# Kernel optimization log

Hardware: AMD Instinct MI355X
Metric: run time of the kernel (lower is better)

## Reference

```python
import jax, jax.numpy as jnp
import numpy as np

B, S, HID, NH, KCLIP = 2, 1500, 1024, 16, 64
HD = HID // NH  # 64


def setup_inputs() -> dict:
    key = jax.random.key(0)
    ks = jax.random.split(key, 16)
    std = 0.02
    inp = {
        "query": jax.random.normal(ks[0], (B, S, HID), jnp.float32),
        "key": jax.random.normal(ks[1], (B, S, HID), jnp.float32),
        "value": jax.random.normal(ks[2], (B, S, HID), jnp.float32),
        # per-head projection weights, stacked over heads: [NH, HID, HD]
        "Wq": jax.random.normal(ks[3], (NH, HID, HD), jnp.float32) * std,
        "bq": jax.random.normal(ks[4], (NH, HD), jnp.float32) * std,
        "Wk": jax.random.normal(ks[5], (NH, HID, HD), jnp.float32) * std,
        "bk": jax.random.normal(ks[6], (NH, HD), jnp.float32) * std,
        "Wv": jax.random.normal(ks[7], (NH, HID, HD), jnp.float32) * std,
        "bv": jax.random.normal(ks[8], (NH, HD), jnp.float32) * std,
        # Shaw relative-position embedding tables: [2k+1, HD]
        "pe_k": jax.random.normal(ks[9], (2 * KCLIP + 1, HD), jnp.float32) * std,
        "pe_v": jax.random.normal(ks[10], (2 * KCLIP + 1, HD), jnp.float32) * std,
        # output projection (torch Linear stored as x @ W + b here)
        "W_fc": jax.random.normal(ks[11], (HID, HID), jnp.float32) * std,
        "b_fc": jax.random.normal(ks[12], (HID,), jnp.float32) * std,
    }
    return inp


def _rel_bias(pe, length, k_clip):
    idx = jnp.arange(length)
    dist = jnp.clip(idx[None, :] - idx[:, None], -k_clip, k_clip) + k_clip
    return pe[dist]  # [S, S, HD]


def reference(query, key, value, Wq, bq, Wk, bk, Wv, bv, pe_k, pe_v, W_fc, b_fc):
    head_dim = Wq.shape[-1]
    seq = query.shape[1]
    k_clip = (pe_k.shape[0] - 1) // 2

    kb = _rel_bias(pe_k, seq, k_clip)  # [S, S, HD]
    vb = _rel_bias(pe_v, seq, k_clip)  # [S, S, HD]

    # batched per-head projections: [B, NH, S, HD]
    Q = jnp.einsum('bsh,nhd->bnsd', query, Wq) + bq[None, :, None, :]
    K = jnp.einsum('bsh,nhd->bnsd', key, Wk) + bk[None, :, None, :]
    V = jnp.einsum('bsh,nhd->bnsd', value, Wv) + bv[None, :, None, :]

    # content term + Shaw relative-key bias term
    scores = jnp.einsum('bnqd,bnkd->bnqk', Q, K) \
           + jnp.einsum('bnqd,qkd->bnqk', Q, kb)
    scores = scores / jnp.sqrt(jnp.asarray(head_dim, scores.dtype))

    w = jax.nn.softmax(scores, axis=-1)  # [B, NH, S, S]

    out = jnp.einsum('bnqk,bnkd->bnqd', w, V) \
        + jnp.einsum('bnqk,qkd->bnqd', w, vb)

    # concat heads (head order matches ModuleList concatenation)
    hidden = out.transpose(0, 2, 1, 3).reshape(query.shape[0], seq, -1)
    return hidden @ W_fc + b_fc
```

## Files before the change

### kernel.cpp

```cpp
#include <hip/hip_runtime.h>
#include <math.h>

#define B_     2
#define S_     1500
#define HID_   1024
#define NH_    16
#define HD_    64
#define M_     (B_*S_)
#define SP_    1536
#define LOG2E  1.4426950408889634f

typedef short bf16x8 __attribute__((ext_vector_type(8)));
typedef short bf16x4 __attribute__((ext_vector_type(4)));
typedef float f32x4  __attribute__((ext_vector_type(4)));

__device__ __forceinline__ float b2f(short s) {
    unsigned u = ((unsigned)(unsigned short)s) << 16;
    return __uint_as_float(u);
}
__device__ __forceinline__ short f2b(float f) {
    unsigned u = __float_as_uint(f);
    unsigned r = (u + 0x7FFFu + ((u >> 16) & 1u)) >> 16;
    return (short)r;
}
__device__ __forceinline__ void gload16(const short* src, short* lds) {
    __builtin_amdgcn_global_load_lds(
        (const __attribute__((address_space(1))) void*)src,
        (__attribute__((address_space(3))) void*)lds, 16, 0, 0);
}

__global__ __launch_bounds__(256) void cvt_act3(
    const float* __restrict__ q, const float* __restrict__ k,
    const float* __restrict__ v, short* __restrict__ oq,
    short* __restrict__ ok, short* __restrict__ ov)
{
    const float* src = blockIdx.y == 0 ? q : blockIdx.y == 1 ? k : v;
    short* dst       = blockIdx.y == 0 ? oq : blockIdx.y == 1 ? ok : ov;
    int i = blockIdx.x * 256 + threadIdx.x;
    const float4* p = (const float4*)(src + (size_t)i * 8);
    float4 a = p[0], b = p[1];
    bf16x8 o;
    o[0]=f2b(a.x); o[1]=f2b(a.y); o[2]=f2b(a.z); o[3]=f2b(a.w);
    o[4]=f2b(b.x); o[5]=f2b(b.y); o[6]=f2b(b.z); o[7]=f2b(b.w);
    *(bf16x8*)(dst + (size_t)i * 8) = o;
}

__global__ __launch_bounds__(256) void prep_w(
    const float* __restrict__ Wq, const float* __restrict__ Wk,
    const float* __restrict__ Wv, const float* __restrict__ Wfc,
    const float* __restrict__ pe_k, const float* __restrict__ pe_v,
    short* __restrict__ Wqt, short* __restrict__ Wkt, short* __restrict__ Wvt,
    short* __restrict__ Wfh, short* __restrict__ Wfl,
    short* __restrict__ pe_kb, short* __restrict__ pe_vt)
{
    int z = blockIdx.x, tid = threadIdx.x;
    if (z == 1024) {
        for (int s = tid; s < 144 * 64; s += 256) {
            int j = s >> 6, d = s & 63;
            pe_kb[s] = (j < 129) ? f2b(pe_k[j * 64 + d]) : (short)0;
        }
        for (int s = tid; s < 64 * 160; s += 256) {
            int d = s / 160, j = s - d * 160;
            pe_vt[s] = (j < 129) ? f2b(pe_v[j * 64 + d]) : (short)0;
        }
        return;
    }
    __shared__ float T[64][65];
    const float* src; short* dhi; short* dlo = nullptr;
    int C, c0, r0; float scale = 1.f;
    if (z < 768) {
        int widx = z >> 8, rem = z & 255;
        int h = rem >> 4, rt = rem & 15;
        src = (widx == 0 ? Wq : widx == 1 ? Wk : Wv) + (size_t)h * 1024 * 64;
        dhi = (widx == 0 ? Wqt : widx == 1 ? Wkt : Wvt) + (size_t)h * 64 * 1024;
        scale = (widx == 0) ? 0.125f * LOG2E : 1.0f;
        C = 64; c0 = 0; r0 = rt * 64;
    } else {
        int idx = z - 768;
        src = Wfc; dhi = Wfh; dlo = Wfl;
        C = 1024; c0 = (idx >> 4) * 64; r0 = (idx & 15) * 64;
    }
#pragma unroll
    for (int i = 0; i < 4; ++i) {
        int slot = tid + i * 256;
        int r = slot >> 4, cg = (slot & 15) * 4;
        float4 v = *(const float4*)(src + (size_t)(r0 + r) * C + c0 + cg);
        T[r][cg+0] = v.x*scale; T[r][cg+1] = v.y*scale;
        T[r][cg+2] = v.z*scale; T[r][cg+3] = v.w*scale;
    }
    __syncthreads();
#pragma unroll
    for (int i = 0; i < 16; ++i) {
        int slot = tid + i * 256;
        int c = slot >> 6, r = slot & 63;
        float v = T[r][c];
        short hi = f2b(v);
        size_t o = (size_t)(c0 + c) * 1024 + r0 + r;
        dhi[o] = hi;
        if (dlo) dlo[o] = f2b(v - b2f(hi));
    }
}

__device__ __forceinline__ void gemm_core(
    const short* __restrict__ Ahi, const short* __restrict__ Alo,
    const short* __restrict__ Bhi, const short* __restrict__ Blo,
    int kIters, int m0, int n0, short* As, short* Bs, f32x4 (&acc)[4][4])
{
    const int tid = threadIdx.x, w = tid >> 6, lane = tid & 63;
    const int l15 = lane & 15, lr4 = lane >> 4;
    const int wr = w >> 1, wc = w & 1;

    for (int it = 0; it < kIters; ++it) {
        int kt = it * 64;
        int seg = kt >> 10, kk0 = kt & 1023;
        const short* Aseg = (seg == 1) ? Alo : Ahi;
        const short* Bseg = (seg == 2) ? Blo : Bhi;
        __syncthreads();
#pragma unroll
        for (int c = 0; c < 4; ++c) {
            int slot = (w * 4 + c) * 64 + lane;
            int r = slot >> 3, cb = slot & 7;
            int sm = m0 + r; sm = sm < M_ ? sm : M_ - 1;
            gload16(Aseg + (size_t)sm * 1024 + kk0 + ((cb ^ (r & 7)) * 8),
                    As + (size_t)(w * 4 + c) * 512);
            gload16(Bseg + (size_t)(n0 + r) * 1024 + kk0 + ((cb ^ (r & 7)) * 8),
                    Bs + (size_t)(w * 4 + c) * 512);
        }
        __syncthreads();
#pragma unroll
        for (int kh = 0; kh < 2; ++kh) {
            bf16x8 aF[4], bF[4];
#pragma unroll
            for (int mi = 0; mi < 4; ++mi) {
                int r = wr * 64 + mi * 16 + l15;
                aF[mi] = *(const bf16x8*)(As + r * 64 + (((kh*4+lr4) ^ (r & 7)) * 8));
            }
#pragma unroll
            for (int ni = 0; ni < 4; ++ni) {
                int r = wc * 64 + ni * 16 + l15;
                bF[ni] = *(const bf16x8*)(Bs + r * 64 + (((kh*4+lr4) ^ (r & 7)) * 8));
            }
#pragma unroll
            for (int mi = 0; mi < 4; ++mi)
#pragma unroll
                for (int ni = 0; ni < 4; ++ni)
                    acc[mi][ni] = __builtin_amdgcn_mfma_f32_16x16x32_bf16(
                        aF[mi], bF[ni], acc[mi][ni], 0, 0, 0);
        }
    }
}

__global__ __launch_bounds__(256) void gemm_qkv(
    const short* __restrict__ qb, const short* __restrict__ kb,
    const short* __restrict__ vb, const short* __restrict__ Wqt,
    const short* __restrict__ Wkt, const short* __restrict__ Wvt,
    const float* __restrict__ bq, const float* __restrict__ bk,
    const float* __restrict__ bv,
    short* __restrict__ Qp, short* __restrict__ Kp, short* __restrict__ Vp)
{
    __shared__ short As[128 * 64];
    __shared__ short Bs[128 * 64];
    const int z = blockIdx.z;
    const short* A  = z == 0 ? qb : z == 1 ? kb : vb;
    const short* Bw = z == 0 ? Wqt : z == 1 ? Wkt : Wvt;
    const float* bias = z == 0 ? bq : z == 1 ? bk : bv;
    const float bscale = z == 0 ? 0.125f * LOG2E : 1.0f;
    short* out = z == 0 ? Qp : z == 1 ? Kp : Vp;
    const int m0 = blockIdx.x * 128, n0 = blockIdx.y * 128;

    f32x4 zf = {0.f,0.f,0.f,0.f};
    f32x4 acc[4][4];
#pragma unroll
    for (int i = 0; i < 4; ++i)
#pragma unroll
        for (int j = 0; j < 4; ++j) acc[i][j] = zf;

    gemm_core(A, A, Bw, Bw, 16, m0, n0, As, Bs, acc);

    const int tid = threadIdx.x, w = tid >> 6, lane = tid & 63;
    const int l15 = lane & 15, lr4 = lane >> 4;
    const int wr = w >> 1, wc = w & 1;
#pragma unroll
    for (int mi = 0; mi < 4; ++mi)
#pragma unroll
        for (int rr = 0; rr < 4; ++rr) {
            int m = m0 + wr * 64 + mi * 16 + lr4 * 4 + rr;
            if (m >= M_) continue;
            int b = m / S_, s = m - b * S_;
#pragma unroll
            for (int ni = 0; ni < 4; ++ni) {
                int n = n0 + wc * 64 + ni * 16 + l15;
                float v = acc[mi][ni][rr] + bias[n] * bscale;
                int h = n >> 6, d = n & 63;
                out[(((size_t)(b * NH_ + h)) * S_ + s) * HD_ + d] = f2b(v);
            }
        }
}

__global__ __launch_bounds__(256) void gemm_fc(
    const short* __restrict__ Ahi, const short* __restrict__ Alo,
    const short* __restrict__ Bhi, const short* __restrict__ Blo,
    const float* __restrict__ bias, float* __restrict__ out)
{
    __shared__ short As[128 * 64];
    __shared__ short Bs[128 * 64];
    const int m0 = blockIdx.x * 128, n0 = blockIdx.y * 128;
    f32x4 zf = {0.f,0.f,0.f,0.f};
    f32x4 acc[4][4];
#pragma unroll
    for (int i = 0; i < 4; ++i)
#pragma unroll
        for (int j = 0; j < 4; ++j) acc[i][j] = zf;

    gemm_core(Ahi, Alo, Bhi, Blo, 32, m0, n0, As, Bs, acc);

    const int tid = threadIdx.x, w = tid >> 6, lane = tid & 63;
    const int l15 = lane & 15, lr4 = lane >> 4;
    const int wr = w >> 1, wc = w & 1;
#pragma unroll
    for (int mi = 0; mi < 4; ++mi)
#pragma unroll
        for (int rr = 0; rr < 4; ++rr) {
            int m = m0 + wr * 64 + mi * 16 + lr4 * 4 + rr;
            if (m >= M_) continue;
#pragma unroll
            for (int ni = 0; ni < 4; ++ni) {
                int n = n0 + wc * 64 + ni * 16 + l15;
                out[(size_t)m * 1024 + n] = acc[mi][ni][rr] + bias[n];
            }
        }
}

__global__ __launch_bounds__(256) void vtrans(
    const short* __restrict__ Vp, short* __restrict__ Vtg)
{
    __shared__ short T[64][72];
    const int bh = blockIdx.y, s0 = blockIdx.x * 64, tid = threadIdx.x;
    const size_t kv = (size_t)bh * S_ * 64;
#pragma unroll
    for (int i = 0; i < 2; ++i) {
        int slot = tid + i * 256;
        int r = slot >> 3, cb = slot & 7;
        int ss = s0 + r; ss = ss < S_ ? ss : S_ - 1;
        bf16x8 v = *(const bf16x8*)(Vp + kv + (size_t)ss * 64 + cb * 8);
        *(bf16x8*)(&T[r][cb * 8]) = v;
    }
    __syncthreads();
#pragma unroll
    for (int i = 0; i < 2; ++i) {
        int slot = tid + i * 256;
        int d = slot >> 3, cg = slot & 7;
        bf16x8 v;
#pragma unroll
        for (int j = 0; j < 8; ++j) {
            int kk = 32 * (cg >> 2) + ((j >> 2) & 1) * 16 + (cg & 3) * 4 + (j & 3);
            v[j] = T[kk][d];
        }
        *(bf16x8*)(Vtg + ((size_t)bh * 64 + d) * SP_ + s0 + cg * 8) = v;
    }
}

__global__ __launch_bounds__(256, 4) void attn_mfma(
    const short* __restrict__ Qb, const short* __restrict__ Kb,
    const short* __restrict__ Vtg, const short* __restrict__ pe_kb,
    const short* __restrict__ pe_vt,
    short* __restrict__ hid_hi, short* __restrict__ hid_lo)
{
    __shared__ short qpe[64 * 144];
    __shared__ short wsm[64 * 160];

    const int tid = threadIdx.x, w = tid >> 6, lane = tid & 63;
    const int l15 = lane & 15, lr4 = lane >> 4;
    const int lg = (blockIdx.x & 7) * 96 + (blockIdx.x >> 3);
    const int bh = lg / 24, bx = lg - bh * 24;
    const int q0 = bx * 64;
    const int qw = q0 + w * 16;
    const int myq = qw + l15;
    const int myrow = w * 16 + l15;
    const size_t kv  = (size_t)bh * S_ * HD_;
    const size_t vtb = (size_t)bh * 64 * SP_;

    {
        short ini = f2b(-1e30f);
        bf16x8 iv;
#pragma unroll
        for (int i = 0; i < 8; ++i) iv[i] = ini;
        short* base = wsm + w * 16 * 160;
#pragma unroll
        for (int i = 0; i < 5; ++i)
            *(bf16x8*)(base + (size_t)(i * 64 + lane) * 8) = iv;
    }

    bf16x8 qA[2];
    {
        int sq = myq < S_ ? myq : S_ - 1;
        const short* qp = Qb + kv + (size_t)sq * 64 + lr4 * 8;
        qA[0] = *(const bf16x8*)(qp);
        qA[1] = *(const bf16x8*)(qp + 32);
    }

    f32x4 zf = {0.f,0.f,0.f,0.f};
#pragma unroll
    for (int jt = 0; jt < 9; ++jt) {
        f32x4 a = zf;
#pragma unroll
        for (int kh = 0; kh < 2; ++kh) {
            bf16x8 pf = *(const bf16x8*)(pe_kb + (size_t)(jt * 16 + l15) * 64 + kh * 32 + lr4 * 8);
            a = __builtin_amdgcn_mfma_f32_16x16x32_bf16(pf, qA[kh], a, 0, 0, 0);
        }
        bf16x4 pk;
#pragma unroll
        for (int rr = 0; rr < 4; ++rr) pk[rr] = f2b(a[rr]);
        *(bf16x4*)(qpe + (size_t)myrow * 144 + jt * 16 + lr4 * 4) = pk;
    }
    const float qpe0   = b2f(qpe[myrow * 144 + 0]);
    const float qpe128 = b2f(qpe[myrow * 144 + 128]);

    float m = 0.f, s0s = 0.f, s1s = 0.f;
    f32x4 o[4];
#pragma unroll
    for (int t = 0; t < 4; ++t) o[t] = zf;

    for (int c = 0; c < 12; ++c) {
        const int kc = c * 128;

        const bool lo0 = (kc +  63 - qw) <= -64, hi0 = (kc       - (qw + 15)) >= 64;
        const bool lo1 = (kc + 127 - qw) <= -64, hi1 = (kc + 64  - (qw + 15)) >= 64;
        const bool mx0 = !(lo0 || hi0), mx1 = !(lo1 || hi1);
        const float ub0 = lo0 ? qpe0 : qpe128;
        const float ub1 = lo1 ? qpe0 : qpe128;

        float rm = -1e30f;
        bf16x8 pa[2][2];
#pragma unroll
        for (int t8 = 0; t8 < 8; ++t8) {
            int sk = kc + t8 * 16 + l15; sk = sk < S_ ? sk : S_ - 1;
            const short* kp = Kb + kv + (size_t)sk * 64 + lr4 * 8;
            bf16x8 k0 = *(const bf16x8*)(kp);
            bf16x8 k1 = *(const bf16x8*)(kp + 32);
            f32x4 s = __builtin_amdgcn_mfma_f32_16x16x32_bf16(k0, qA[0], zf, 0, 0, 0);
            s = __builtin_amdgcn_mfma_f32_16x16x32_bf16(k1, qA[1], s, 0, 0, 0);

            const int h = t8 >> 2, tt = t8 & 3;
            const int wn = tt >> 1, sl = (tt & 1) * 4;
            const bool mx = h ? mx1 : mx0;
            const bool alo = h ? lo1 : lo0;
            const float ub = h ? ub1 : ub0;
#pragma unroll
            for (int rr = 0; rr < 4; ++rr) {
                int k = kc + t8 * 16 + lr4 * 4 + rr;
                int rel = k - myq;
                float v;
                if (mx) {
                    int jc = rel < -64 ? 0 : (rel > 64 ? 128 : rel + 64);
                    v = s[rr] + b2f(qpe[myrow * 144 + jc]);
                } else {
                    v = s[rr] + ub;
                }
                if (k >= S_) v = -1e30f;
                rm = fmaxf(rm, v);
                if (mx && rel > -64 && rel < 64)
                    wsm[myrow * 160 + rel + 64] = f2b(v);
                float p2 = exp2f(v - m);
                pa[h][wn][sl + rr] = f2b(p2);
                if (mx) {
                    if (rel <= -64) s0s += p2; else if (rel >= 64) s1s += p2;
                } else if (alo) s0s += p2; else s1s += p2;
            }
        }

        __builtin_amdgcn_s_setprio(1);
#pragma unroll
        for (int h = 0; h < 2; ++h)
#pragma unroll
            for (int wn = 0; wn < 2; ++wn)
#pragma unroll
                for (int td = 0; td < 4; ++td) {
                    int r = td * 16 + l15;
                    int cbv = h * 8 + wn * 4 + lr4;
                    bf16x8 vB = *(const bf16x8*)(Vtg + vtb + (size_t)r * SP_ + kc + cbv * 8);
                    o[td] = __builtin_amdgcn_mfma_f32_16x16x32_bf16(pa[h][wn], vB, o[td], 0, 0, 0);
                }
        __builtin_amdgcn_s_setprio(0);

        rm = fmaxf(rm, __shfl_xor(rm, 16));
        rm = fmaxf(rm, __shfl_xor(rm, 32));
        if (!__all(rm <= m + 8.f)) {
            float nm = fmaxf(m, rm);
            float fac = exp2f(m - nm);
            m = nm; s0s *= fac; s1s *= fac;
            float fo[4];
#pragma unroll
            for (int rr = 0; rr < 4; ++rr) fo[rr] = __shfl(fac, lr4 * 4 + rr);
#pragma unroll
            for (int t = 0; t < 4; ++t)
#pragma unroll
                for (int rr = 0; rr < 4; ++rr) o[t][rr] *= fo[rr];
        }
    }

    s0s += __shfl_xor(s0s, 16); s0s += __shfl_xor(s0s, 32);
    s1s += __shfl_xor(s1s, 16); s1s += __shfl_xor(s1s, 32);

    short* rowp = wsm + (size_t)myrow * 160;
    float midsum = 0.f;
#pragma unroll
    for (int cc = 0; cc < 5; ++cc) {
        int off = (cc * 4 + lr4) * 8;
        bf16x8 mv = *(const bf16x8*)(rowp + off);
        bf16x8 ev;
#pragma unroll
        for (int jj = 0; jj < 8; ++jj) {
            float e = exp2f(b2f(mv[jj]) - m);
            ev[jj] = f2b(e);
            midsum += e;
        }
        *(bf16x8*)(rowp + off) = ev;
    }
    midsum += __shfl_xor(midsum, 16); midsum += __shfl_xor(midsum, 32);
    const float linv = 1.f / (s0s + s1s + midsum);
    if (lr4 == 0) { rowp[0] = f2b(s0s); rowp[128] = f2b(s1s); }

#pragma unroll
    for (int jh = 0; jh < 5; ++jh) {
        bf16x8 aW = *(const bf16x8*)(wsm + (size_t)myrow * 160 + jh * 32 + lr4 * 8);
#pragma unroll
        for (int td = 0; td < 4; ++td) {
            bf16x8 bW = *(const bf16x8*)(pe_vt + (size_t)(td * 16 + l15) * 160 + jh * 32 + lr4 * 8);
            o[td] = __builtin_amdgcn_mfma_f32_16x16x32_bf16(aW, bW, o[td], 0, 0, 0);
        }
    }

    {
        float fo[4];
#pragma unroll
        for (int rr = 0; rr < 4; ++rr) fo[rr] = __shfl(linv, lr4 * 4 + rr);
#pragma unroll
        for (int td = 0; td < 4; ++td)
#pragma unroll
            for (int rr = 0; rr < 4; ++rr) o[td][rr] *= fo[rr];
    }

#pragma unroll
    for (int td = 0; td < 4; ++td)
#pragma unroll
        for (int rr = 0; rr < 4; ++rr) {
            int qrow = lr4 * 4 + rr;
            int d = td * 16 + l15;
            int inner = (((d >> 2) ^ ((qrow & 7) << 1)) << 2) + (d & 3);
            float v = o[td][rr];
            short hi = f2b(v);
            wsm[(w * 16 + qrow) * 160 + inner] = hi;
            qpe[(w * 16 + qrow) * 144 + inner] = f2b(v - b2f(hi));
        }
    {
        int b = bh >> 4, h = bh & 15;
        int qrow = lane >> 2;
        int q = q0 + w * 16 + qrow;
#pragma unroll
        for (int i = 0; i < 2; ++i) {
            int cb = (lane & 3) * 2 + i;
            int qws = (cb * 2) ^ ((qrow & 7) << 1);
            bf16x8 hv = *(const bf16x8*)(wsm + (w * 16 + qrow) * 160 + qws * 4);
            bf16x8 lv = *(const bf16x8*)(qpe + (w * 16 + qrow) * 144 + qws * 4);
            if (q < S_) {
                size_t oo = ((size_t)(b * S_ + q)) * 1024 + h * 64 + cb * 8;
                *(bf16x8*)(hid_hi + oo) = hv;
                *(bf16x8*)(hid_lo + oo) = lv;
            }
        }
    }
}

extern "C" void kernel_launch(void* const* d_in, const int* in_sizes, int n_in,
                              void* d_out, int out_size, void* d_ws, size_t ws_size,
                              hipStream_t stream)
{
    const float* query = (const float*)d_in[0];
    const float* key   = (const float*)d_in[1];
    const float* value = (const float*)d_in[2];
    const float* Wq    = (const float*)d_in[3];
    const float* bq    = (const float*)d_in[4];
    const float* Wk    = (const float*)d_in[5];
    const float* bk    = (const float*)d_in[6];
    const float* Wv    = (const float*)d_in[7];
    const float* bv    = (const float*)d_in[8];
    const float* pe_k  = (const float*)d_in[9];
    const float* pe_v  = (const float*)d_in[10];
    const float* W_fc  = (const float*)d_in[11];
    const float* b_fc  = (const float*)d_in[12];

    char* W = (char*)d_ws;
    short* qb   = (short*)(W + 0);
    short* kb   = (short*)(W + 6291456);
    short* vb   = (short*)(W + 12582912);
    short* Vtg  = vb;
    short* Wqt  = (short*)(W + 18874368);
    short* Wkt  = (short*)(W + 20971520);
    short* Wvt  = (short*)(W + 23068672);
    short* Wfh  = (short*)(W + 25165824);
    short* Wfl  = (short*)(W + 27262976);
    short* Qp   = (short*)(W + 29360128);
    short* Kp   = (short*)(W + 35651584);
    short* Vp   = (short*)(W + 41943040);
    short* pekb = (short*)(W + 48234496);
    short* pevt = (short*)(W + 48252928);
    short* hidh = qb;
    short* hidl = kb;

    cvt_act3<<<dim3(1500, 3), 256, 0, stream>>>(query, key, value, qb, kb, vb);
    prep_w<<<1025, 256, 0, stream>>>(Wq, Wk, Wv, W_fc, pe_k, pe_v,
                                     Wqt, Wkt, Wvt, Wfh, Wfl, pekb, pevt);
    gemm_qkv<<<dim3(24, 8, 3), 256, 0, stream>>>(qb, kb, vb, Wqt, Wkt, Wvt,
                                                 bq, bk, bv, Qp, Kp, Vp);
    vtrans<<<dim3(24, 32), 256, 0, stream>>>(Vp, Vtg);
    attn_mfma<<<768, 256, 0, stream>>>(Qp, Kp, Vtg, pekb, pevt, hidh, hidl);
    gemm_fc<<<dim3(24, 8), 256, 0, stream>>>(hidh, hidl, Wfh, Wfl, b_fc, (float*)d_out);
}
```

Measured before the change: 267.0 us.

## Process two 16-row query tiles per wave to reuse K and V fragments

The attention kernel now uses 128-thread blocks where each wave handles 32 query rows as two 16-row MFMA tiles. Each K fragment and V fragment loaded from global memory feeds two MFMAs instead of one, halving K/V load traffic per query. The cost is roughly doubled accumulator and probability registers per wave and fewer waves per block, which may lower occupancy and latency hiding. The launch bounds hint that fixed 4 blocks per CU was also dropped.

```diff
diff --git a/kernel.cpp b/kernel.cpp
--- a/kernel.cpp
+++ b/kernel.cpp
@@ -260,7 +260,7 @@
     }
 }
 
-__global__ __launch_bounds__(256, 4) void attn_mfma(
+__global__ __launch_bounds__(128) void attn_mfma(
     const short* __restrict__ Qb, const short* __restrict__ Kb,
     const short* __restrict__ Vtg, const short* __restrict__ pe_kb,
     const short* __restrict__ pe_vt,
@@ -274,98 +274,125 @@
     const int lg = (blockIdx.x & 7) * 96 + (blockIdx.x >> 3);
     const int bh = lg / 24, bx = lg - bh * 24;
     const int q0 = bx * 64;
-    const int qw = q0 + w * 16;
-    const int myq = qw + l15;
-    const int myrow = w * 16 + l15;
+    const int qwave = q0 + w * 32;
     const size_t kv  = (size_t)bh * S_ * HD_;
     const size_t vtb = (size_t)bh * 64 * SP_;
+
+    int myq[2], myrow[2];
+#pragma unroll
+    for (int t2 = 0; t2 < 2; ++t2) {
+        myq[t2] = qwave + t2 * 16 + l15;
+        myrow[t2] = w * 32 + t2 * 16 + l15;
+    }
 
     {
         short ini = f2b(-1e30f);
         bf16x8 iv;
 #pragma unroll
         for (int i = 0; i < 8; ++i) iv[i] = ini;
-        short* base = wsm + w * 16 * 160;
-#pragma unroll
-        for (int i = 0; i < 5; ++i)
+        short* base = wsm + w * 32 * 160;
+#pragma unroll
+        for (int i = 0; i < 10; ++i)
             *(bf16x8*)(base + (size_t)(i * 64 + lane) * 8) = iv;
     }
 
-    bf16x8 qA[2];
-    {
-        int sq = myq < S_ ? myq : S_ - 1;
+    bf16x8 qA[2][2];
+#pragma unroll
+    for (int t2 = 0; t2 < 2; ++t2) {
+        int sq = myq[t2] < S_ ? myq[t2] : S_ - 1;
         const short* qp = Qb + kv + (size_t)sq * 64 + lr4 * 8;
-        qA[0] = *(const bf16x8*)(qp);
-        qA[1] = *(const bf16x8*)(qp + 32);
+        qA[t2][0] = *(const bf16x8*)(qp);
+        qA[t2][1] = *(const bf16x8*)(qp + 32);
     }
 
     f32x4 zf = {0.f,0.f,0.f,0.f};
 #pragma unroll
-    for (int jt = 0; jt < 9; ++jt) {
-        f32x4 a = zf;
-#pragma unroll
-        for (int kh = 0; kh < 2; ++kh) {
-            bf16x8 pf = *(const bf16x8*)(pe_kb + (size_t)(jt * 16 + l15) * 64 + kh * 32 + lr4 * 8);
-            a = __builtin_amdgcn_mfma_f32_16x16x32_bf16(pf, qA[kh], a, 0, 0, 0);
-        }
-        bf16x4 pk;
-#pragma unroll
-        for (int rr = 0; rr < 4; ++rr) pk[rr] = f2b(a[rr]);
-        *(bf16x4*)(qpe + (size_t)myrow * 144 + jt * 16 + lr4 * 4) = pk;
-    }
-    const float qpe0   = b2f(qpe[myrow * 144 + 0]);
-    const float qpe128 = b2f(qpe[myrow * 144 + 128]);
-
-    float m = 0.f, s0s = 0.f, s1s = 0.f;
-    f32x4 o[4];
-#pragma unroll
-    for (int t = 0; t < 4; ++t) o[t] = zf;
+    for (int t2 = 0; t2 < 2; ++t2)
+#pragma unroll
+        for (int jt = 0; jt < 9; ++jt) {
+            f32x4 a = zf;
+#pragma unroll
+            for (int kh = 0; kh < 2; ++kh) {
+                bf16x8 pf = *(const bf16x8*)(pe_kb + (size_t)(jt * 16 + l15) * 64 + kh * 32 + lr4 * 8);
+                a = __builtin_amdgcn_mfma_f32_16x16x32_bf16(pf, qA[t2][kh], a, 0, 0, 0);
+            }
+            bf16x4 pk;
+#pragma unroll
+            for (int rr = 0; rr < 4; ++rr) pk[rr] = f2b(a[rr]);
+            *(bf16x4*)(qpe + (size_t)myrow[t2] * 144 + jt * 16 + lr4 * 4) = pk;
+        }
+    float qpe0[2], qpe128[2];
+#pragma unroll
+    for (int t2 = 0; t2 < 2; ++t2) {
+        qpe0[t2]   = b2f(qpe[myrow[t2] * 144 + 0]);
+        qpe128[t2] = b2f(qpe[myrow[t2] * 144 + 128]);
+    }
+
+    float m[2] = {0.f, 0.f}, s0s[2] = {0.f, 0.f}, s1s[2] = {0.f, 0.f};
+    f32x4 o[2][4];
+#pragma unroll
+    for (int t2 = 0; t2 < 2; ++t2)
+#pragma unroll
+        for (int t = 0; t < 4; ++t) o[t2][t] = zf;
 
     for (int c = 0; c < 12; ++c) {
         const int kc = c * 128;
 
-        const bool lo0 = (kc +  63 - qw) <= -64, hi0 = (kc       - (qw + 15)) >= 64;
-        const bool lo1 = (kc + 127 - qw) <= -64, hi1 = (kc + 64  - (qw + 15)) >= 64;
-        const bool mx0 = !(lo0 || hi0), mx1 = !(lo1 || hi1);
-        const float ub0 = lo0 ? qpe0 : qpe128;
-        const float ub1 = lo1 ? qpe0 : qpe128;
-
-        float rm = -1e30f;
-        bf16x8 pa[2][2];
+        bool mx[2][2], alo[2][2];
+        float ub[2][2];
+#pragma unroll
+        for (int t2 = 0; t2 < 2; ++t2) {
+            int qt = qwave + t2 * 16;
+#pragma unroll
+            for (int h = 0; h < 2; ++h) {
+                bool lo = (kc + h * 64 + 63 - qt) <= -64;
+                bool hi = (kc + h * 64 - (qt + 15)) >= 64;
+                mx[t2][h] = !(lo || hi);
+                alo[t2][h] = lo;
+                ub[t2][h] = lo ? qpe0[t2] : qpe128[t2];
+            }
+        }
+
+        float rm[2] = {-1e30f, -1e30f};
+        bf16x8 pa[2][2][2];
 #pragma unroll
         for (int t8 = 0; t8 < 8; ++t8) {
             int sk = kc + t8 * 16 + l15; sk = sk < S_ ? sk : S_ - 1;
             const short* kp = Kb + kv + (size_t)sk * 64 + lr4 * 8;
             bf16x8 k0 = *(const bf16x8*)(kp);
             bf16x8 k1 = *(const bf16x8*)(kp + 32);
-            f32x4 s = __builtin_amdgcn_mfma_f32_16x16x32_bf16(k0, qA[0], zf, 0, 0, 0);
-            s = __builtin_amdgcn_mfma_f32_16x16x32_bf16(k1, qA[1], s, 0, 0, 0);
-
             const int h = t8 >> 2, tt = t8 & 3;
             const int wn = tt >> 1, sl = (tt & 1) * 4;
-            const bool mx = h ? mx1 : mx0;
-            const bool alo = h ? lo1 : lo0;
-            const float ub = h ? ub1 : ub0;
-#pragma unroll
-            for (int rr = 0; rr < 4; ++rr) {
-                int k = kc + t8 * 16 + lr4 * 4 + rr;
-                int rel = k - myq;
-                float v;
-                if (mx) {
-                    int jc = rel < -64 ? 0 : (rel > 64 ? 128 : rel + 64);
-                    v = s[rr] + b2f(qpe[myrow * 144 + jc]);
-                } else {
-                    v = s[rr] + ub;
+#pragma unroll
+            for (int t2 = 0; t2 < 2; ++t2) {
+                f32x4 s = __builtin_amdgcn_mfma_f32_16x16x32_bf16(k0, qA[t2][0], zf, 0, 0, 0);
+                s = __builtin_amdgcn_mfma_f32_16x16x32_bf16(k1, qA[t2][1], s, 0, 0, 0);
+                const bool mxx = mx[t2][h];
+                const bool aloo = alo[t2][h];
+                const float ubb = ub[t2][h];
+#pragma unroll
+                for (int rr = 0; rr < 4; ++rr) {
+                    int k = kc + t8 * 16 + lr4 * 4 + rr;
+                    int rel = k - myq[t2];
+                    float v;
+                    if (mxx) {
+                        int jc = rel < -64 ? 0 : (rel > 64 ? 128 : rel + 64);
+                        v = s[rr] + b2f(qpe[myrow[t2] * 144 + jc]);
+                    } else {
+                        v = s[rr] + ubb;
+                    }
+                    if (k >= S_) v = -1e30f;
+                    rm[t2] = fmaxf(rm[t2], v);
+                    if (mxx && rel > -64 && rel < 64)
+                        wsm[myrow[t2] * 160 + rel + 64] = f2b(v);
+                    float p2 = exp2f(v - m[t2]);
+                    pa[t2][h][wn][sl + rr] = f2b(p2);
+                    if (mxx) {
+                        if (rel <= -64) s0s[t2] += p2;
+                        else if (rel >= 64) s1s[t2] += p2;
+                    } else if (aloo) s0s[t2] += p2;
+                    else s1s[t2] += p2;
                 }
-                if (k >= S_) v = -1e30f;
-                rm = fmaxf(rm, v);
-                if (mx && rel > -64 && rel < 64)
-                    wsm[myrow * 160 + rel + 64] = f2b(v);
-                float p2 = exp2f(v - m);
-                pa[h][wn][sl + rr] = f2b(p2);
-                if (mx) {
-                    if (rel <= -64) s0s += p2; else if (rel >= 64) s1s += p2;
-                } else if (alo) s0s += p2; else s1s += p2;
             }
         }
 
@@ -378,95 +405,107 @@
                 for (int td = 0; td < 4; ++td) {
                     int r = td * 16 + l15;
                     int cbv = h * 8 + wn * 4 + lr4;
-                    bf16x8 vB = *(const bf16x8*)(Vtg + vtb + (size_t)r * SP_ + kc + cbv * 8);
-                    o[td] = __builtin_amdgcn_mfma_f32_16x16x32_bf16(pa[h][wn], vB, o[td], 0, 0, 0);
+                    bf16x8 vB = *(const bf16x8*)(
+                        Vtg + vtb + (size_t)r * SP_ + kc + cbv * 8);
+                    o[0][td] = __builtin_amdgcn_mfma_f32_16x16x32_bf16(
+                        pa[0][h][wn], vB, o[0][td], 0, 0, 0);
+                    o[1][td] = __builtin_amdgcn_mfma_f32_16x16x32_bf16(
+                        pa[1][h][wn], vB, o[1][td], 0, 0, 0);
                 }
         __builtin_amdgcn_s_setprio(0);
 
-        rm = fmaxf(rm, __shfl_xor(rm, 16));
-        rm = fmaxf(rm, __shfl_xor(rm, 32));
-        if (!__all(rm <= m + 8.f)) {
-            float nm = fmaxf(m, rm);
-            float fac = exp2f(m - nm);
-            m = nm; s0s *= fac; s1s *= fac;
+#pragma unroll
+        for (int t2 = 0; t2 < 2; ++t2) {
+            float r2 = rm[t2];
+            r2 = fmaxf(r2, __shfl_xor(r2, 16));
+            r2 = fmaxf(r2, __shfl_xor(r2, 32));
+            if (!__all(r2 <= m[t2] + 8.f)) {
+                float nm = fmaxf(m[t2], r2);
+                float fac = exp2f(m[t2] - nm);
+                m[t2] = nm; s0s[t2] *= fac; s1s[t2] *= fac;
+                float fo[4];
+#pragma unroll
+                for (int rr = 0; rr < 4; ++rr) fo[rr] = __shfl(fac, lr4 * 4 + rr);
+#pragma unroll
+                for (int t = 0; t < 4; ++t)
+#pragma unroll
+                    for (int rr = 0; rr < 4; ++rr) o[t2][t][rr] *= fo[rr];
+            }
+        }
+    }
+
+#pragma unroll
+    for (int t2 = 0; t2 < 2; ++t2) {
+        float s0 = s0s[t2], s1 = s1s[t2], mm = m[t2];
+        s0 += __shfl_xor(s0, 16); s0 += __shfl_xor(s0, 32);
+        s1 += __shfl_xor(s1, 16); s1 += __shfl_xor(s1, 32);
+
+        short* rowp = wsm + (size_t)myrow[t2] * 160;
+        float midsum = 0.f;
+#pragma unroll
+        for (int cc = 0; cc < 5; ++cc) {
+            int off = (cc * 4 + lr4) * 8;
+            bf16x8 mv = *(const bf16x8*)(rowp + off);
+            bf16x8 ev;
+#pragma unroll
+            for (int jj = 0; jj < 8; ++jj) {
+                float e = exp2f(b2f(mv[jj]) - mm);
+                ev[jj] = f2b(e);
+                midsum += e;
+            }
+            *(bf16x8*)(rowp + off) = ev;
+        }
+        midsum += __shfl_xor(midsum, 16); midsum += __shfl_xor(midsum, 32);
+        const float linv = 1.f / (s0 + s1 + midsum);
+        if (lr4 == 0) { rowp[0] = f2b(s0); rowp[128] = f2b(s1); }
+
+#pragma unroll
+        for (int jh = 0; jh < 5; ++jh) {
+            bf16x8 aW = *(const bf16x8*)(wsm + (size_t)myrow[t2] * 160 + jh * 32 + lr4 * 8);
+#pragma unroll
+            for (int td = 0; td < 4; ++td) {
+                bf16x8 bW = *(const bf16x8*)(pe_vt + (size_t)(td * 16 + l15) * 160 + jh * 32 + lr4 * 8);
+                o[t2][td] = __builtin_amdgcn_mfma_f32_16x16x32_bf16(aW, bW, o[t2][td], 0, 0, 0);
+            }
+        }
+
+        {
             float fo[4];
 #pragma unroll
-            for (int rr = 0; rr < 4; ++rr) fo[rr] = __shfl(fac, lr4 * 4 + rr);
-#pragma unroll
-            for (int t = 0; t < 4; ++t)
-#pragma unroll
-                for (int rr = 0; rr < 4; ++rr) o[t][rr] *= fo[rr];
-        }
-    }
-
-    s0s += __shfl_xor(s0s, 16); s0s += __shfl_xor(s0s, 32);
-    s1s += __shfl_xor(s1s, 16); s1s += __shfl_xor(s1s, 32);
-
-    short* rowp = wsm + (size_t)myrow * 160;
-    float midsum = 0.f;
-#pragma unroll
-    for (int cc = 0; cc < 5; ++cc) {
-        int off = (cc * 4 + lr4) * 8;
-        bf16x8 mv = *(const bf16x8*)(rowp + off);
-        bf16x8 ev;
-#pragma unroll
-        for (int jj = 0; jj < 8; ++jj) {
-            float e = exp2f(b2f(mv[jj]) - m);
-            ev[jj] = f2b(e);
-            midsum += e;
-        }
-        *(bf16x8*)(rowp + off) = ev;
-    }
-    midsum += __shfl_xor(midsum, 16); midsum += __shfl_xor(midsum, 32);
-    const float linv = 1.f / (s0s + s1s + midsum);
-    if (lr4 == 0) { rowp[0] = f2b(s0s); rowp[128] = f2b(s1s); }
-
-#pragma unroll
-    for (int jh = 0; jh < 5; ++jh) {
-        bf16x8 aW = *(const bf16x8*)(wsm + (size_t)myrow * 160 + jh * 32 + lr4 * 8);
-#pragma unroll
-        for (int td = 0; td < 4; ++td) {
-            bf16x8 bW = *(const bf16x8*)(pe_vt + (size_t)(td * 16 + l15) * 160 + jh * 32 + lr4 * 8);
-            o[td] = __builtin_amdgcn_mfma_f32_16x16x32_bf16(aW, bW, o[td], 0, 0, 0);
-        }
-    }
-
-    {
-        float fo[4];
-#pragma unroll
-        for (int rr = 0; rr < 4; ++rr) fo[rr] = __shfl(linv, lr4 * 4 + rr);
+            for (int rr = 0; rr < 4; ++rr) fo[rr] = __shfl(linv, lr4 * 4 + rr);
+#pragma unroll
+            for (int td = 0; td < 4; ++td)
+#pragma unroll
+                for (int rr = 0; rr < 4; ++rr) o[t2][td][rr] *= fo[rr];
+        }
+
 #pragma unroll
         for (int td = 0; td < 4; ++td)
 #pragma unroll
-            for (int rr = 0; rr < 4; ++rr) o[td][rr] *= fo[rr];
-    }
-
-#pragma unroll
-    for (int td = 0; td < 4; ++td)
-#pragma unroll
-        for (int rr = 0; rr < 4; ++rr) {
-            int qrow = lr4 * 4 + rr;
-            int d = td * 16 + l15;
-            int inner = (((d >> 2) ^ ((qrow & 7) << 1)) << 2) + (d & 3);
-            float v = o[td][rr];
-            short hi = f2b(v);
-            wsm[(w * 16 + qrow) * 160 + inner] = hi;
-            qpe[(w * 16 + qrow) * 144 + inner] = f2b(v - b2f(hi));
-        }
-    {
-        int b = bh >> 4, h = bh & 15;
-        int qrow = lane >> 2;
-        int q = q0 + w * 16 + qrow;
-#pragma unroll
-        for (int i = 0; i < 2; ++i) {
-            int cb = (lane & 3) * 2 + i;
-            int qws = (cb * 2) ^ ((qrow & 7) << 1);
-            bf16x8 hv = *(const bf16x8*)(wsm + (w * 16 + qrow) * 160 + qws * 4);
-            bf16x8 lv = *(const bf16x8*)(qpe + (w * 16 + qrow) * 144 + qws * 4);
-            if (q < S_) {
-                size_t oo = ((size_t)(b * S_ + q)) * 1024 + h * 64 + cb * 8;
-                *(bf16x8*)(hid_hi + oo) = hv;
-                *(bf16x8*)(hid_lo + oo) = lv;
+            for (int rr = 0; rr < 4; ++rr) {
+                int qrow = lr4 * 4 + rr;
+                int d = td * 16 + l15;
+                int inner = (((d >> 2) ^ ((qrow & 7) << 1)) << 2) + (d & 3);
+                float v = o[t2][td][rr];
+                short hi = f2b(v);
+                wsm[(w * 32 + t2 * 16 + qrow) * 160 + inner] = hi;
+                qpe[(w * 32 + t2 * 16 + qrow) * 144 + inner] = f2b(v - b2f(hi));
+            }
+        {
+            int b = bh >> 4, h = bh & 15;
+            int qrow = lane >> 2;
+            int q = qwave + t2 * 16 + qrow;
+#pragma unroll
+            for (int i = 0; i < 2; ++i) {
+                int cb = (lane & 3) * 2 + i;
+                int qws = (cb * 2) ^ ((qrow & 7) << 1);
+                bf16x8 hv = *(const bf16x8*)(wsm + (w * 32 + t2 * 16 + qrow) * 160 + qws * 4);
+                bf16x8 lv = *(const bf16x8*)(qpe + (w * 32 + t2 * 16 + qrow) * 144 + qws * 4);
+                if (q < S_) {
+                    size_t oo = ((size_t)(b * S_ + q)) * 1024 + h * 64 + cb * 8;
+                    *(bf16x8*)(hid_hi + oo) = hv;
+                    *(bf16x8*)(hid_lo + oo) = lv;
+                }
             }
         }
     }
@@ -514,6 +553,6 @@
     gemm_qkv<<<dim3(24, 8, 3), 256, 0, stream>>>(qb, kb, vb, Wqt, Wkt, Wvt,
                                                  bq, bk, bv, Qp, Kp, Vp);
     vtrans<<<dim3(24, 32), 256, 0, stream>>>(Vp, Vtg);
-    attn_mfma<<<768, 256, 0, stream>>>(Qp, Kp, Vtg, pekb, pevt, hidh, hidl);
+    attn_mfma<<<768, 128, 0, stream>>>(Qp, Kp, Vtg, pekb, pevt, hidh, hidl);
     gemm_fc<<<dim3(24, 8), 256, 0, stream>>>(hidh, hidl, Wfh, Wfl, b_fc, (float*)d_out);
 }
```

New measurement: 277.9 us. 1.04x slower.
